# Performance work log

Measured on AMD Instinct MI355X. Metric: run time of the kernel, lower is better.

Reference implementation:

```python
import jax, jax.numpy as jnp
import numpy as np

B, N, FE, CIN, COUT, H = 4, 256, 8, 16, 16, 64


def setup_inputs() -> dict:
    key = jax.random.key(0)
    k0, k1, k2, k3, k4 = jax.random.split(key, 5)
    node_attr = jax.random.normal(k0, (B, N, CIN), dtype=jnp.float32)
    edge_adj = jax.random.normal(k1, (B, N, N, FE), dtype=jnp.float32)
    # edge-network MLP: FE -> H (ReLU) -> CIN*COUT
    W1 = jax.random.normal(k2, (FE, H), dtype=jnp.float32) * (1.0 / np.sqrt(FE))
    b1 = jnp.zeros((H,), dtype=jnp.float32)
    W2 = jax.random.normal(k3, (H, CIN * COUT), dtype=jnp.float32) * (1.0 / np.sqrt(H))
    b2 = jnp.zeros((CIN * COUT,), dtype=jnp.float32)
    bound = 1.0 / np.sqrt(CIN)
    root = jax.random.uniform(k4, (CIN, COUT), dtype=jnp.float32, minval=-bound, maxval=bound)
    return {"node_attr": node_attr, "edge_adj": edge_adj, "W1": W1, "b1": b1,
            "W2": W2, "b2": b2, "root": root}


def reference(node_attr, edge_adj, W1, b1, W2, b2, root):
    b, n = edge_adj.shape[0], edge_adj.shape[1]
    cin, cout = root.shape
    fe = edge_adj.shape[-1]
    # net over all N^2 edge features -> per-edge [Cin, Cout] weight matrices
    e = edge_adj.reshape(b, n * n, fe)
    h = jax.nn.relu(e @ W1 + b1)                       # [B, N*N, H]
    w = (h @ W2 + b2).reshape(b, n, n, cin, cout)      # [B, i, j, Cin, Cout]
    # gather index = scatter index = (k mod N): edge (i,j) reads node j,
    # scatter-sums into node j  =>  out[j] = sum_i x[j] @ W[i, j]
    msg = jnp.einsum('bjc,bijcd->bijd', node_attr, w)  # [B, i, j, Cout]
    out = msg.sum(axis=1)                              # [B, N, Cout]
    out = out + node_attr @ root                       # root/self term
    return out
```

## Files before the change

### kernel.cpp

```cpp
#include <hip/hip_runtime.h>

#define B_    4
#define N_    256
#define FE_   8
#define CIN_  16
#define COUT_ 16
#define H_    64
#define S_    32


__global__ __launch_bounds__(256) void k1_partial_hsum(
    const float* __restrict__ edge_adj,
    const float* __restrict__ W1,
    const float* __restrict__ b1,
    float* __restrict__ partial)
{
    const int blk = blockIdx.x;
    const int s   = blk >> 4;
    const int b   = (blk >> 2) & 3;
    const int jt  = blk & 3;
    const int t    = threadIdx.x;
    const int lane = t & 63;
    const int w    = t >> 6;

    __shared__ float bufA[64][H_ + 1];
    __shared__ float bufB[64][H_ + 1];

    const int i0 = s * 8 + w * 2;
    const int j  = jt * 64 + lane;
    const float* e0p = edge_adj + (((size_t)b * N_ + i0)     * N_ + j) * FE_;
    const float* e1p = edge_adj + (((size_t)b * N_ + i0 + 1) * N_ + j) * FE_;
    const float4 e0a = ((const float4*)e0p)[0];
    const float4 e0b = ((const float4*)e0p)[1];
    const float4 e1a = ((const float4*)e1p)[0];
    const float4 e1b = ((const float4*)e1p)[1];

    float acc[H_];
    #pragma unroll
    for (int h = 0; h < H_; ++h) {
        const float w0 = W1[0 * H_ + h];
        const float w1 = W1[1 * H_ + h];
        const float w2 = W1[2 * H_ + h];
        const float w3 = W1[3 * H_ + h];
        const float w4 = W1[4 * H_ + h];
        const float w5 = W1[5 * H_ + h];
        const float w6 = W1[6 * H_ + h];
        const float w7 = W1[7 * H_ + h];
        const float bb = b1[h];

        float v0 = bb, v1 = bb;
        v0 = fmaf(e0a.x, w0, v0);  v1 = fmaf(e1a.x, w0, v1);
        v0 = fmaf(e0a.y, w1, v0);  v1 = fmaf(e1a.y, w1, v1);
        v0 = fmaf(e0a.z, w2, v0);  v1 = fmaf(e1a.z, w2, v1);
        v0 = fmaf(e0a.w, w3, v0);  v1 = fmaf(e1a.w, w3, v1);
        v0 = fmaf(e0b.x, w4, v0);  v1 = fmaf(e1b.x, w4, v1);
        v0 = fmaf(e0b.y, w5, v0);  v1 = fmaf(e1b.y, w5, v1);
        v0 = fmaf(e0b.z, w6, v0);  v1 = fmaf(e1b.z, w6, v1);
        v0 = fmaf(e0b.w, w7, v0);  v1 = fmaf(e1b.w, w7, v1);

        acc[h] = fmaxf(v0, 0.f) + fmaxf(v1, 0.f);
    }

    float (*mybuf)[H_ + 1] = (w < 2) ? bufA : bufB;
    if ((w & 1) == 0) {
        #pragma unroll
        for (int h = 0; h < H_; ++h) mybuf[lane][h] = acc[h];
    }
    __syncthreads();
    if ((w & 1) == 1) {
        #pragma unroll
        for (int h = 0; h < H_; ++h) mybuf[lane][h] += acc[h];
    }
    __syncthreads();

    float* dst = partial + (size_t)blk * (64 * H_);
    #pragma unroll
    for (int k = 0; k < 16; ++k) {
        const int cell = k * 256 + t;
        const int jj   = cell >> 6;
        const int h    = cell & 63;
        dst[cell] = bufA[jj][h] + bufB[jj][h];
    }
}

__global__ __launch_bounds__(256) void k2_output(
    const float* __restrict__ node_attr,
    const float* __restrict__ W2,
    const float* __restrict__ b2,
    const float* __restrict__ root,
    const float* __restrict__ partial,
    float* __restrict__ out)
{
    const int bj = blockIdx.x;
    const int b  = bj >> 8;
    const int j  = bj & (N_ - 1);
    const int jt = j >> 6;
    const int jj = j & 63;
    const int t  = threadIdx.x;

    __shared__ float sp[4][H_];
    __shared__ float Hsum[H_];
    __shared__ float contrib[CIN_][COUT_];

    {
        const int sw = t >> 6;
        const int h  = t & 63;
        float a = 0.f;
        #pragma unroll
        for (int k = 0; k < 8; ++k) {
            const int s = sw + k * 4;
            a += partial[(((size_t)(s * 16 + b * 4 + jt)) * 64 + jj) * 64 + h];
        }
        sp[sw][h] = a;
    }
    __syncthreads();
    if (t < H_) Hsum[t] = sp[0][t] + sp[1][t] + sp[2][t] + sp[3][t];
    __syncthreads();

    float ws = (float)N_ * b2[t];
    #pragma unroll 8
    for (int h = 0; h < H_; ++h) {
        ws = fmaf(Hsum[h], W2[h * (CIN_ * COUT_) + t], ws);
    }

    const int c = t >> 4;
    const int d = t & 15;
    const float nodec = node_attr[((size_t)b * N_ + j) * CIN_ + c];
    contrib[c][d] = nodec * (ws + root[t]);
    __syncthreads();

    if (t < COUT_) {
        float o = 0.f;
        #pragma unroll
        for (int cc = 0; cc < CIN_; ++cc) o += contrib[cc][t];
        out[((size_t)b * N_ + j) * COUT_ + t] = o;
    }
}

extern "C" void kernel_launch(void* const* d_in, const int* in_sizes, int n_in,
                              void* d_out, int out_size, void* d_ws, size_t ws_size,
                              hipStream_t stream) {
    const float* node_attr = (const float*)d_in[0];
    const float* edge_adj  = (const float*)d_in[1];
    const float* W1        = (const float*)d_in[2];
    const float* b1        = (const float*)d_in[3];
    const float* W2        = (const float*)d_in[4];
    const float* b2        = (const float*)d_in[5];
    const float* root      = (const float*)d_in[6];
    float* out = (float*)d_out;

    float* partial = (float*)d_ws;

    k1_partial_hsum<<<dim3(S_ * B_ * 4), dim3(256), 0, stream>>>(
        edge_adj, W1, b1, partial);
    k2_output<<<dim3(B_ * N_), dim3(256), 0, stream>>>(
        node_attr, W2, b2, root, partial, out);
}
```

Measured before the change: 85.44 us.

## Pack W1 rows, transpose partial layout, process four nodes per output block

Adds a tiny kernel that packs W1 and b1 into a padded per-hidden-unit row layout, so k1 reads each unit's weights contiguously. The partial buffer is re-laid out as [b, j, s, h], which lets k2 read it with contiguous float4 loads. k2 now handles four nodes per block and reuses each W2 load across them, cutting W2 traffic and block count by four. The cost is one extra kernel launch, and k1's global stores become strided across s.

```diff
diff --git a/kernel.cpp b/kernel.cpp
--- a/kernel.cpp
+++ b/kernel.cpp
@@ -9,10 +9,24 @@
 #define S_    32
 
 
+__global__ __launch_bounds__(256) void k0_pack_w1(
+    const float* __restrict__ W1,
+    const float* __restrict__ b1,
+    float* __restrict__ W1t)
+{
+    const int t = threadIdx.x;
+    for (int idx = t; idx < H_ * 16; idx += 256) {
+        const int h = idx >> 4, f = idx & 15;
+        float v = 0.f;
+        if (f < FE_)       v = W1[f * H_ + h];
+        else if (f == FE_) v = b1[h];
+        W1t[idx] = v;
+    }
+}
+
 __global__ __launch_bounds__(256) void k1_partial_hsum(
     const float* __restrict__ edge_adj,
-    const float* __restrict__ W1,
-    const float* __restrict__ b1,
+    const float* __restrict__ W1t,
     float* __restrict__ partial)
 {
     const int blk = blockIdx.x;
@@ -38,15 +52,10 @@
     float acc[H_];
     #pragma unroll
     for (int h = 0; h < H_; ++h) {
-        const float w0 = W1[0 * H_ + h];
-        const float w1 = W1[1 * H_ + h];
-        const float w2 = W1[2 * H_ + h];
-        const float w3 = W1[3 * H_ + h];
-        const float w4 = W1[4 * H_ + h];
-        const float w5 = W1[5 * H_ + h];
-        const float w6 = W1[6 * H_ + h];
-        const float w7 = W1[7 * H_ + h];
-        const float bb = b1[h];
+        const float* wrow = W1t + h * 16;
+        const float w0 = wrow[0], w1 = wrow[1], w2 = wrow[2], w3 = wrow[3];
+        const float w4 = wrow[4], w5 = wrow[5], w6 = wrow[6], w7 = wrow[7];
+        const float bb = wrow[8];
 
         float v0 = bb, v1 = bb;
         v0 = fmaf(e0a.x, w0, v0);  v1 = fmaf(e1a.x, w0, v1);
@@ -73,13 +82,11 @@
     }
     __syncthreads();
 
-    float* dst = partial + (size_t)blk * (64 * H_);
     #pragma unroll
     for (int k = 0; k < 16; ++k) {
-        const int cell = k * 256 + t;
-        const int jj   = cell >> 6;
-        const int h    = cell & 63;
-        dst[cell] = bufA[jj][h] + bufB[jj][h];
+        const int jj = w * 16 + k;
+        const float v = bufA[jj][lane] + bufB[jj][lane];
+        partial[(((size_t)b * N_ + jt * 64 + jj) * S_ + s) * 64 + lane] = v;
     }
 }
 
@@ -91,49 +98,72 @@
     const float* __restrict__ partial,
     float* __restrict__ out)
 {
-    const int bj = blockIdx.x;
-    const int b  = bj >> 8;
-    const int j  = bj & (N_ - 1);
-    const int jt = j >> 6;
-    const int jj = j & 63;
-    const int t  = threadIdx.x;
+    const int blk = blockIdx.x;
+    const int b   = blk >> 6;
+    const int jg  = (blk & 63) * 4;
+    const int t    = threadIdx.x;
+    const int jl   = t >> 6;
+    const int lane = t & 63;
 
-    __shared__ float sp[4][H_];
-    __shared__ float Hsum[H_];
-    __shared__ float contrib[CIN_][COUT_];
+    __shared__ float sred[4][4][64];
+    __shared__ float Hs4[4][H_];
+    __shared__ float con[4][CIN_][COUT_];
 
     {
-        const int sw = t >> 6;
-        const int h  = t & 63;
-        float a = 0.f;
+        const int sg = lane >> 4;
+        const int h0 = (lane & 15) << 2;
+        const float* base = partial + ((size_t)(b * N_ + jg + jl) * S_) * 64;
+        float4 a4 = make_float4(0.f, 0.f, 0.f, 0.f);
         #pragma unroll
         for (int k = 0; k < 8; ++k) {
-            const int s = sw + k * 4;
-            a += partial[(((size_t)(s * 16 + b * 4 + jt)) * 64 + jj) * 64 + h];
+            const float4 v = *(const float4*)(base + (sg * 8 + k) * 64 + h0);
+            a4.x += v.x; a4.y += v.y; a4.z += v.z; a4.w += v.w;
         }
-        sp[sw][h] = a;
+        *(float4*)(&sred[jl][sg][h0]) = a4;
     }
     __syncthreads();
-    if (t < H_) Hsum[t] = sp[0][t] + sp[1][t] + sp[2][t] + sp[3][t];
+    Hs4[jl][lane] = sred[jl][0][lane] + sred[jl][1][lane]
+                  + sred[jl][2][lane] + sred[jl][3][lane];
     __syncthreads();
 
-    float ws = (float)N_ * b2[t];
-    #pragma unroll 8
-    for (int h = 0; h < H_; ++h) {
-        ws = fmaf(Hsum[h], W2[h * (CIN_ * COUT_) + t], ws);
+    float ws0 = (float)N_ * b2[t];
+    float ws1 = ws0, ws2 = ws0, ws3 = ws0;
+    #pragma unroll
+    for (int hq = 0; hq < 16; ++hq) {
+        const int hh = hq * 4;
+        const float4 hv0 = *(const float4*)(&Hs4[0][hh]);
+        const float4 hv1 = *(const float4*)(&Hs4[1][hh]);
+        const float4 hv2 = *(const float4*)(&Hs4[2][hh]);
+        const float4 hv3 = *(const float4*)(&Hs4[3][hh]);
+        const float wv0 = W2[(hh + 0) * 256 + t];
+        const float wv1 = W2[(hh + 1) * 256 + t];
+        const float wv2 = W2[(hh + 2) * 256 + t];
+        const float wv3 = W2[(hh + 3) * 256 + t];
+        ws0 = fmaf(hv0.x, wv0, ws0); ws0 = fmaf(hv0.y, wv1, ws0);
+        ws0 = fmaf(hv0.z, wv2, ws0); ws0 = fmaf(hv0.w, wv3, ws0);
+        ws1 = fmaf(hv1.x, wv0, ws1); ws1 = fmaf(hv1.y, wv1, ws1);
+        ws1 = fmaf(hv1.z, wv2, ws1); ws1 = fmaf(hv1.w, wv3, ws1);
+        ws2 = fmaf(hv2.x, wv0, ws2); ws2 = fmaf(hv2.y, wv1, ws2);
+        ws2 = fmaf(hv2.z, wv2, ws2); ws2 = fmaf(hv2.w, wv3, ws2);
+        ws3 = fmaf(hv3.x, wv0, ws3); ws3 = fmaf(hv3.y, wv1, ws3);
+        ws3 = fmaf(hv3.z, wv2, ws3); ws3 = fmaf(hv3.w, wv3, ws3);
     }
 
-    const int c = t >> 4;
-    const int d = t & 15;
-    const float nodec = node_attr[((size_t)b * N_ + j) * CIN_ + c];
-    contrib[c][d] = nodec * (ws + root[t]);
+    {
+        const int c = t >> 4, d = t & 15;
+        const float rt = root[t];
+        con[0][c][d] = node_attr[((size_t)(b * N_ + jg + 0)) * CIN_ + c] * (ws0 + rt);
+        con[1][c][d] = node_attr[((size_t)(b * N_ + jg + 1)) * CIN_ + c] * (ws1 + rt);
+        con[2][c][d] = node_attr[((size_t)(b * N_ + jg + 2)) * CIN_ + c] * (ws2 + rt);
+        con[3][c][d] = node_attr[((size_t)(b * N_ + jg + 3)) * CIN_ + c] * (ws3 + rt);
+    }
     __syncthreads();
-
-    if (t < COUT_) {
+    if (t < 64) {
+        const int jl2 = t >> 4, d = t & 15;
         float o = 0.f;
         #pragma unroll
-        for (int cc = 0; cc < CIN_; ++cc) o += contrib[cc][t];
-        out[((size_t)b * N_ + j) * COUT_ + t] = o;
+        for (int cc = 0; cc < CIN_; ++cc) o += con[jl2][cc][d];
+        out[((size_t)(b * N_ + jg + jl2)) * COUT_ + d] = o;
     }
 }
 
@@ -149,10 +179,12 @@
     const float* root      = (const float*)d_in[6];
     float* out = (float*)d_out;
 
-    float* partial = (float*)d_ws;
+    float* W1t     = (float*)d_ws;
+    float* partial = (float*)((char*)d_ws + 4096);
 
+    k0_pack_w1<<<dim3(1), dim3(256), 0, stream>>>(W1, b1, W1t);
     k1_partial_hsum<<<dim3(S_ * B_ * 4), dim3(256), 0, stream>>>(
-        edge_adj, W1, b1, partial);
-    k2_output<<<dim3(B_ * N_), dim3(256), 0, stream>>>(
+        edge_adj, W1t, partial);
+    k2_output<<<dim3(B_ * N_ / 4), dim3(256), 0, stream>>>(
         node_attr, W2, b2, root, partial, out);
 }
```

Result: slower. 99.43 us (+16.4%).
